# Kernel tuning notes

Measured on AMD Instinct MI355X. Metric: run time of the kernel, lower is better.

Reference implementation:

```python
import jax, jax.numpy as jnp
import numpy as np

B, D1, DJ, S, OUT = 8, 1024, 512, 2048, 2048
IN = D1 + 2 * DJ  # linear input_dim = 2048


def setup_inputs() -> dict:
    key = jax.random.key(0)
    k1, k2, k3, kw, kb = jax.random.split(key, 5)
    return {
        "input1": jax.random.normal(k1, (B, D1, S), dtype=jnp.float32),
        "input2_a": jax.random.normal(k2, (B, DJ, S), dtype=jnp.float32),
        "input2_b": jax.random.normal(k3, (B, DJ, S), dtype=jnp.float32),
        "W": jax.random.normal(kw, (OUT, IN), dtype=jnp.float32) * (1.0 / np.sqrt(IN)),
        "b": jax.random.normal(kb, (OUT,), dtype=jnp.float32) * 0.01,
    }


def reference(input1, input2_a, input2_b, W, b):
    # Original loops over seq_len, per-step concat along feature dim then linear.
    # Fused: concat along feature axis once, transpose to [B, S, F], one GEMM.
    x = jnp.concatenate([input1, input2_a, input2_b], axis=1)  # [B, IN, S]
    x = jnp.transpose(x, (0, 2, 1))                            # [B, S, IN]
    out = jnp.einsum('bsf,of->bso', x, W) + b                  # [B, S, OUT]
    return out
```

## Files before the change

kernel.cpp:

```cpp
#include <hip/hip_runtime.h>
#include <hip/hip_bf16.h>

#define B_   8
#define D1_  1024
#define DJ_  512
#define S_   2048
#define OUT_ 2048
#define IN_  2048
#define M_TOT (B_ * S_)

typedef __attribute__((ext_vector_type(8))) short          bf16x8;
typedef __attribute__((ext_vector_type(8))) unsigned short ushort8;
typedef __attribute__((ext_vector_type(4))) float          f32x4;

typedef __attribute__((address_space(3))) unsigned int as3_uint;
typedef __attribute__((address_space(1))) unsigned int as1_uint;

__device__ __forceinline__ unsigned short f2bf(float f) {
    union { float f; unsigned u; } v; v.f = f;
    unsigned r = v.u + 0x7FFF + ((v.u >> 16) & 1);
    return (unsigned short)(r >> 16);
}

__device__ __forceinline__ void gload_lds16(const void* g, const void* l) {
    __builtin_amdgcn_global_load_lds(
        (const as1_uint*)(unsigned long long)g,
        (as3_uint*)(unsigned int)(unsigned long long)l,
        16, 0, 0);
}

__global__ __launch_bounds__(256) void prep_kernel(
        const float* __restrict__ in1, const float* __restrict__ in2a,
        const float* __restrict__ in2b, const float* __restrict__ W,
        unsigned short* __restrict__ Xt, unsigned short* __restrict__ Wb) {
    int bid = blockIdx.x;
    if (bid >= 8192) {
        size_t i = (size_t)(bid - 8192) * 256 + threadIdx.x;
        const float4* p = reinterpret_cast<const float4*>(W) + i * 2;
        float4 a = p[0], c = p[1];
        ushort8 h;
        h[0] = f2bf(a.x); h[1] = f2bf(a.y); h[2] = f2bf(a.z); h[3] = f2bf(a.w);
        h[4] = f2bf(c.x); h[5] = f2bf(c.y); h[6] = f2bf(c.z); h[7] = f2bf(c.w);
        *(reinterpret_cast<ushort8*>(Wb) + i) = h;
        return;
    }
    __shared__ float tile[64][65];
    int st = bid & 31;
    int ft = (bid >> 5) & 31;
    int b  = bid >> 10;
    int f0 = ft << 6, s0 = st << 6;

    const float* src; int frel;
    if (f0 < D1_)             { src = in1  + (size_t)b * D1_ * S_; frel = f0; }
    else if (f0 < D1_ + DJ_)  { src = in2a + (size_t)b * DJ_ * S_; frel = f0 - D1_; }
    else                      { src = in2b + (size_t)b * DJ_ * S_; frel = f0 - (D1_ + DJ_); }

    int t = threadIdx.x;
    int tr = t >> 4, tc = t & 15;
    #pragma unroll
    for (int i = 0; i < 4; ++i) {
        int fi = tr + i * 16;
        const float4 v = *reinterpret_cast<const float4*>(
            &src[(size_t)(frel + fi) * S_ + s0 + tc * 4]);
        tile[fi][tc * 4 + 0] = v.x; tile[fi][tc * 4 + 1] = v.y;
        tile[fi][tc * 4 + 2] = v.z; tile[fi][tc * 4 + 3] = v.w;
    }
    __syncthreads();
    int si0 = t >> 3, fx = t & 7;
    #pragma unroll
    for (int i = 0; i < 2; ++i) {
        int si = si0 + i * 32;
        ushort8 h;
        #pragma unroll
        for (int j = 0; j < 8; ++j) h[j] = f2bf(tile[fx * 8 + j][si]);
        *reinterpret_cast<ushort8*>(
            &Xt[(size_t)(b * S_ + s0 + si) * IN_ + f0 + fx * 8]) = h;
    }
}


__global__ __launch_bounds__(512, 2) void gemm256_kernel(
        const unsigned short* __restrict__ A,
        const unsigned short* __restrict__ Bm,
        const float* __restrict__ bias,
        float* __restrict__ C) {
    __shared__ unsigned short As_[32768];
    __shared__ unsigned short Bs_[32768];

    int bid = blockIdx.x;
    int swz = (bid & 7) * 64 + (bid >> 3);
    int m0 = (swz >> 3) * 256;
    int n0 = (swz & 7) * 256;

    int t = threadIdx.x;
    int lane = t & 63, wave = t >> 6;
    int wm = wave >> 2;
    int wn = wave & 3;
    int fr = lane & 15;
    int fkslot = lane >> 4;

    int sr  = t >> 3;
    int sc  = t & 7;
    int swc = sc ^ (sr & 7);

    int sl0 = ((fkslot)     ^ (fr & 7)) * 8;
    int sl1 = ((4 + fkslot) ^ (fr & 7)) * 8;
    int arow = wm * 64 + fr;
    int brow = wn * 32 + fr;

#define STAGE_A(bb, h, kt) do { \
    const unsigned short* _g0 = A + (size_t)(m0 + (h)*64 + sr) * IN_ + (kt) + swc*8; \
    const unsigned short* _g1 = A + (size_t)(m0 + 128 + (h)*64 + sr) * IN_ + (kt) + swc*8; \
    unsigned short* _l = As_ + ((bb)*2 + (h))*8192 + sr*64 + sc*8; \
    gload_lds16(_g0, _l); \
    gload_lds16(_g1, _l + 4096); \
} while (0)

#define STAGE_B(bb, h, kt) do { \
    const unsigned short* _g0 = Bm + (size_t)(n0 + (sr>>5)*64 + (h)*32 + (sr&31)) * IN_ + (kt) + swc*8; \
    const unsigned short* _g1 = Bm + (size_t)(n0 + 128 + (sr>>5)*64 + (h)*32 + (sr&31)) * IN_ + (kt) + swc*8; \
    unsigned short* _l = Bs_ + ((bb)*2 + (h))*8192 + sr*64 + sc*8; \
    gload_lds16(_g0, _l); \
    gload_lds16(_g1, _l + 4096); \
} while (0)

#define READ_A(bb, qm) do { \
    const unsigned short* _Ab = As_ + ((bb)*2 + (qm))*8192; \
    _Pragma("unroll") \
    for (int i = 0; i < 4; ++i) { \
        int rr = (arow + i*16) * 64; \
        a_[i][0] = *reinterpret_cast<const bf16x8*>(_Ab + rr + sl0); \
        a_[i][1] = *reinterpret_cast<const bf16x8*>(_Ab + rr + sl1); \
    } \
} while (0)

#define READ_B(bb, qn, DST) do { \
    const unsigned short* _Bb = Bs_ + ((bb)*2 + (qn))*8192; \
    _Pragma("unroll") \
    for (int j = 0; j < 2; ++j) { \
        int rr = (brow + j*16) * 64; \
        DST[j][0] = *reinterpret_cast<const bf16x8*>(_Bb + rr + sl0); \
        DST[j][1] = *reinterpret_cast<const bf16x8*>(_Bb + rr + sl1); \
    } \
} while (0)

#define MFMA4(qm, qn, BS) \
    _Pragma("unroll") \
    for (int i = 0; i < 4; ++i) { \
        _Pragma("unroll") \
        for (int j = 0; j < 2; ++j) { \
            acc[(qm)*4+i][(qn)*2+j] = __builtin_amdgcn_mfma_f32_16x16x32_bf16( \
                a_[i][0], BS[j][0], acc[(qm)*4+i][(qn)*2+j], 0, 0, 0); \
            acc[(qm)*4+i][(qn)*2+j] = __builtin_amdgcn_mfma_f32_16x16x32_bf16( \
                a_[i][1], BS[j][1], acc[(qm)*4+i][(qn)*2+j], 0, 0, 0); \
        } \
    }

#define LGKM0 do { \
    asm volatile("s_waitcnt lgkmcnt(0)" ::: "memory"); \
    __builtin_amdgcn_sched_barrier(0); \
} while (0)

#define VMW asm volatile("s_waitcnt vmcnt(4)" ::: "memory")

#define SP_EVEN(bb, S1, S2, VM_STMT) do { \
    READ_B(bb, 0, b0_); \
    READ_A(bb, 0); \
    S1; S2; \
    LGKM0; \
    __builtin_amdgcn_s_setprio(1); \
    MFMA4(0, 0, b0_) \
    __builtin_amdgcn_s_setprio(0); \
    READ_B(bb, 1, b1_); \
    LGKM0; \
    __builtin_amdgcn_s_setprio(1); \
    MFMA4(0, 1, b1_) \
    __builtin_amdgcn_s_setprio(0); \
    VM_STMT; \
    __builtin_amdgcn_s_barrier(); \
} while (0)

#define SP_ODD(bb, S1, S2, VM_STMT) do { \
    READ_A(bb, 1); \
    S1; S2; \
    LGKM0; \
    __builtin_amdgcn_s_setprio(1); \
    MFMA4(1, 1, b1_) \
    MFMA4(1, 0, b0_) \
    __builtin_amdgcn_s_setprio(0); \
    VM_STMT; \
    __builtin_amdgcn_s_barrier(); \
} while (0)

    f32x4 acc[8][4] = {};
    bf16x8 a_[4][2], b0_[2][2], b1_[2][2];

    STAGE_A(0, 0, 0);  STAGE_A(0, 1, 0);
    STAGE_B(0, 0, 0);  STAGE_B(0, 1, 0);
    STAGE_A(1, 0, 64); STAGE_B(1, 1, 64);
    asm volatile("s_waitcnt vmcnt(4)" ::: "memory");
    __builtin_amdgcn_s_barrier();

    for (int it = 0; it < IN_ / 128; ++it) {
        int k1 = it * 128 + 64;
        int k2 = (it * 128 + 128) & (IN_ - 1);
        int k3 = (it * 128 + 192) & (IN_ - 1);
        SP_EVEN(0, STAGE_A(1, 1, k1), STAGE_B(1, 0, k1), );
        SP_ODD (0, STAGE_A(0, 0, k2), STAGE_B(0, 1, k2), VMW);
        SP_EVEN(1, STAGE_A(0, 1, k2), STAGE_B(0, 0, k2), );
        SP_ODD (1, STAGE_A(1, 0, k3), STAGE_B(1, 1, k3), VMW);
    }

    float bv[4];
    #pragma unroll
    for (int n_ = 0; n_ < 4; ++n_) bv[n_] = bias[n0 + wn * 64 + n_ * 16 + fr];
    int crow0 = m0 + wm * 128 + (lane >> 4) * 4;
    int ccol0 = n0 + wn * 64 + fr;
    #pragma unroll
    for (int mi = 0; mi < 8; ++mi) {
        #pragma unroll
        for (int r_ = 0; r_ < 4; ++r_) {
            float* cp = C + (size_t)(crow0 + mi * 16 + r_) * OUT_ + ccol0;
            #pragma unroll
            for (int n_ = 0; n_ < 4; ++n_) cp[n_ * 16] = acc[mi][n_][r_] + bv[n_];
        }
    }
#undef STAGE_A
#undef STAGE_B
#undef READ_A
#undef READ_B
#undef MFMA4
#undef LGKM0
#undef VMW
#undef SP_EVEN
#undef SP_ODD
}

__global__ __launch_bounds__(256) void naive_kernel(
        const float* __restrict__ in1, const float* __restrict__ in2a,
        const float* __restrict__ in2b, const float* __restrict__ W,
        const float* __restrict__ bias, float* __restrict__ out) {
    size_t id = (size_t)blockIdx.x * 256 + threadIdx.x;
    int s = (int)(id & (S_ - 1));
    size_t bo = id >> 11;
    int o = (int)(bo & (OUT_ - 1));
    int b = (int)(bo >> 11);
    const float* w = W + (size_t)o * IN_;
    float acc = bias[o];
    const float* x1 = in1 + (size_t)b * D1_ * S_ + s;
    for (int f = 0; f < D1_; ++f) acc += x1[(size_t)f * S_] * w[f];
    const float* x2 = in2a + (size_t)b * DJ_ * S_ + s;
    for (int f = 0; f < DJ_; ++f) acc += x2[(size_t)f * S_] * w[D1_ + f];
    const float* x3 = in2b + (size_t)b * DJ_ * S_ + s;
    for (int f = 0; f < DJ_; ++f) acc += x3[(size_t)f * S_] * w[D1_ + DJ_ + f];
    out[((size_t)b * S_ + s) * OUT_ + o] = acc;
}

extern "C" void kernel_launch(void* const* d_in, const int* in_sizes, int n_in,
                              void* d_out, int out_size, void* d_ws, size_t ws_size,
                              hipStream_t stream) {
    const float* in1  = (const float*)d_in[0];
    const float* in2a = (const float*)d_in[1];
    const float* in2b = (const float*)d_in[2];
    const float* W    = (const float*)d_in[3];
    const float* bias = (const float*)d_in[4];
    float* out = (float*)d_out;

    const size_t xt_bytes = (size_t)M_TOT * IN_ * 2;
    const size_t wb_bytes = (size_t)OUT_ * IN_ * 2;

    if (ws_size < xt_bytes + wb_bytes) {
        naive_kernel<<<(B_ * (size_t)OUT_ * S_) / 256, 256, 0, stream>>>(
            in1, in2a, in2b, W, bias, out);
        return;
    }

    unsigned short* Xt = (unsigned short*)d_ws;
    unsigned short* Wb = (unsigned short*)((char*)d_ws + xt_bytes);

    prep_kernel<<<8192 + (OUT_ * IN_) / (256 * 8), 256, 0, stream>>>(
        in1, in2a, in2b, W, Xt, Wb);
    gemm256_kernel<<<(M_TOT / 256) * (OUT_ / 256), 512, 0, stream>>>(Xt, Wb, bias, out);
}
```

Baseline: 159.9 us.

## Switch GEMM inner MFMA from 16x16x32 to 32x32x16 bf16 tiles

Replaces the 16x16x32 MFMA tiles with 32x32x16 bf16 MFMAs. Each wave now computes 4x2 32x32 accumulator blocks instead of 8x4 16x16 ones. The LDS read pattern, swizzle indexing and epilogue store mapping are rewritten to match the 32x32 lane layout. The intent is fewer MFMA instructions and fewer LDS fragment reads per k-step, which means less issue overhead and better operand reuse. In exchange, the epilogue store pattern changes to 32-column strided writes.

```diff
diff --git a/kernel.cpp b/kernel.cpp
--- a/kernel.cpp
+++ b/kernel.cpp
@@ -9,9 +9,9 @@
 #define IN_  2048
 #define M_TOT (B_ * S_)
 
-typedef __attribute__((ext_vector_type(8))) short          bf16x8;
-typedef __attribute__((ext_vector_type(8))) unsigned short ushort8;
-typedef __attribute__((ext_vector_type(4))) float          f32x4;
+typedef __attribute__((ext_vector_type(8)))  short          bf16x8;
+typedef __attribute__((ext_vector_type(8)))  unsigned short ushort8;
+typedef __attribute__((ext_vector_type(16))) float          f32x16;
 
 typedef __attribute__((address_space(3))) unsigned int as3_uint;
 typedef __attribute__((address_space(1))) unsigned int as1_uint;
@@ -96,17 +96,17 @@
     int lane = t & 63, wave = t >> 6;
     int wm = wave >> 2;
     int wn = wave & 3;
-    int fr = lane & 15;
-    int fkslot = lane >> 4;
+    int lane31 = lane & 31;
+    int khi    = lane >> 5;
 
     int sr  = t >> 3;
     int sc  = t & 7;
     int swc = sc ^ (sr & 7);
 
-    int sl0 = ((fkslot)     ^ (fr & 7)) * 8;
-    int sl1 = ((4 + fkslot) ^ (fr & 7)) * 8;
-    int arow = wm * 64 + fr;
-    int brow = wn * 32 + fr;
+    int alr0 = wm * 64 + lane31;
+    int asw  = alr0 & 7;
+    int blr  = wn * 32 + lane31;
+    int bsw  = blr & 7;
 
 #define STAGE_A(bb, h, kt) do { \
     const unsigned short* _g0 = A + (size_t)(m0 + (h)*64 + sr) * IN_ + (kt) + swc*8; \
@@ -124,36 +124,33 @@
     gload_lds16(_g1, _l + 4096); \
 } while (0)
 
-#define READ_A(bb, qm) do { \
+#define READ_A2(bb, qm) do { \
     const unsigned short* _Ab = As_ + ((bb)*2 + (qm))*8192; \
     _Pragma("unroll") \
-    for (int i = 0; i < 4; ++i) { \
-        int rr = (arow + i*16) * 64; \
-        a_[i][0] = *reinterpret_cast<const bf16x8*>(_Ab + rr + sl0); \
-        a_[i][1] = *reinterpret_cast<const bf16x8*>(_Ab + rr + sl1); \
+    for (int ii = 0; ii < 2; ++ii) { \
+        int _base = (alr0 + ii*32) * 64; \
+        _Pragma("unroll") \
+        for (int kk = 0; kk < 4; ++kk) \
+            a_[ii][kk] = *reinterpret_cast<const bf16x8*>( \
+                _Ab + _base + (((kk*2 + khi) ^ asw) * 8)); \
     } \
 } while (0)
 
-#define READ_B(bb, qn, DST) do { \
+#define READ_B32(bb, qn, DST) do { \
     const unsigned short* _Bb = Bs_ + ((bb)*2 + (qn))*8192; \
     _Pragma("unroll") \
-    for (int j = 0; j < 2; ++j) { \
-        int rr = (brow + j*16) * 64; \
-        DST[j][0] = *reinterpret_cast<const bf16x8*>(_Bb + rr + sl0); \
-        DST[j][1] = *reinterpret_cast<const bf16x8*>(_Bb + rr + sl1); \
-    } \
-} while (0)
-
-#define MFMA4(qm, qn, BS) \
+    for (int kk = 0; kk < 4; ++kk) \
+        DST[kk] = *reinterpret_cast<const bf16x8*>( \
+            _Bb + blr*64 + (((kk*2 + khi) ^ bsw) * 8)); \
+} while (0)
+
+#define MFMA8(qm, qn, BS) \
     _Pragma("unroll") \
-    for (int i = 0; i < 4; ++i) { \
+    for (int ii = 0; ii < 2; ++ii) { \
         _Pragma("unroll") \
-        for (int j = 0; j < 2; ++j) { \
-            acc[(qm)*4+i][(qn)*2+j] = __builtin_amdgcn_mfma_f32_16x16x32_bf16( \
-                a_[i][0], BS[j][0], acc[(qm)*4+i][(qn)*2+j], 0, 0, 0); \
-            acc[(qm)*4+i][(qn)*2+j] = __builtin_amdgcn_mfma_f32_16x16x32_bf16( \
-                a_[i][1], BS[j][1], acc[(qm)*4+i][(qn)*2+j], 0, 0, 0); \
-        } \
+        for (int kk = 0; kk < 4; ++kk) \
+            acc32[(qm)*2+ii][qn] = __builtin_amdgcn_mfma_f32_32x32x16_bf16( \
+                a_[ii][kk], BS[kk], acc32[(qm)*2+ii][qn], 0, 0, 0); \
     }
 
 #define LGKM0 do { \
@@ -164,36 +161,36 @@
 #define VMW asm volatile("s_waitcnt vmcnt(4)" ::: "memory")
 
 #define SP_EVEN(bb, S1, S2, VM_STMT) do { \
-    READ_B(bb, 0, b0_); \
-    READ_A(bb, 0); \
+    READ_B32(bb, 0, bq0_); \
+    READ_A2(bb, 0); \
     S1; S2; \
     LGKM0; \
     __builtin_amdgcn_s_setprio(1); \
-    MFMA4(0, 0, b0_) \
+    MFMA8(0, 0, bq0_) \
     __builtin_amdgcn_s_setprio(0); \
-    READ_B(bb, 1, b1_); \
+    READ_B32(bb, 1, bq1_); \
     LGKM0; \
     __builtin_amdgcn_s_setprio(1); \
-    MFMA4(0, 1, b1_) \
+    MFMA8(0, 1, bq1_) \
     __builtin_amdgcn_s_setprio(0); \
     VM_STMT; \
     __builtin_amdgcn_s_barrier(); \
 } while (0)
 
 #define SP_ODD(bb, S1, S2, VM_STMT) do { \
-    READ_A(bb, 1); \
+    READ_A2(bb, 1); \
     S1; S2; \
     LGKM0; \
     __builtin_amdgcn_s_setprio(1); \
-    MFMA4(1, 1, b1_) \
-    MFMA4(1, 0, b0_) \
+    MFMA8(1, 1, bq1_) \
+    MFMA8(1, 0, bq0_) \
     __builtin_amdgcn_s_setprio(0); \
     VM_STMT; \
     __builtin_amdgcn_s_barrier(); \
 } while (0)
 
-    f32x4 acc[8][4] = {};
-    bf16x8 a_[4][2], b0_[2][2], b1_[2][2];
+    f32x16 acc32[4][2] = {};
+    bf16x8 a_[2][4], bq0_[4], bq1_[4];
 
     STAGE_A(0, 0, 0);  STAGE_A(0, 1, 0);
     STAGE_B(0, 0, 0);  STAGE_B(0, 1, 0);
@@ -211,25 +208,30 @@
         SP_ODD (1, STAGE_A(1, 0, k3), STAGE_B(1, 1, k3), VMW);
     }
 
-    float bv[4];
-    #pragma unroll
-    for (int n_ = 0; n_ < 4; ++n_) bv[n_] = bias[n0 + wn * 64 + n_ * 16 + fr];
-    int crow0 = m0 + wm * 128 + (lane >> 4) * 4;
-    int ccol0 = n0 + wn * 64 + fr;
-    #pragma unroll
-    for (int mi = 0; mi < 8; ++mi) {
+    float bv2[2];
+    #pragma unroll
+    for (int qn = 0; qn < 2; ++qn) bv2[qn] = bias[n0 + wn * 64 + qn * 32 + lane31];
+    int crow0 = m0 + wm * 128 + 4 * khi;
+    int ccol0 = n0 + wn * 64 + lane31;
+    #pragma unroll
+    for (int it2 = 0; it2 < 4; ++it2) {
         #pragma unroll
-        for (int r_ = 0; r_ < 4; ++r_) {
-            float* cp = C + (size_t)(crow0 + mi * 16 + r_) * OUT_ + ccol0;
+        for (int rq = 0; rq < 4; ++rq) {
             #pragma unroll
-            for (int n_ = 0; n_ < 4; ++n_) cp[n_ * 16] = acc[mi][n_][r_] + bv[n_];
+            for (int rr = 0; rr < 4; ++rr) {
+                int row = crow0 + it2 * 32 + rq * 8 + rr;
+                int reg = rq * 4 + rr;
+                float* cp = C + (size_t)row * OUT_ + ccol0;
+                cp[0]  = acc32[it2][0][reg] + bv2[0];
+                cp[32] = acc32[it2][1][reg] + bv2[1];
+            }
         }
     }
 #undef STAGE_A
 #undef STAGE_B
-#undef READ_A
-#undef READ_B
-#undef MFMA4
+#undef READ_A2
+#undef READ_B32
+#undef MFMA8
 #undef LGKM0
 #undef VMW
 #undef SP_EVEN
```

Result: slower. 175.9 us (+10.0%).
